# Performance work log

Hardware: AMD Instinct MI355X
Metric: run time of the kernel (lower is better)

Reference implementation:

```python
import jax, jax.numpy as jnp
import numpy as np

D = 256; NH = 8; NL = 4; NP = 4; DH = D // NH; DFFN = 1024; NQ = 900; BS = 4
SPATIAL = ((92, 92), (46, 46), (23, 23), (12, 12))  # (H, W) per level
LEVEL_START = (0, 8464, 10580, 11109)
S = sum(h * w for h, w in SPATIAL)  # 11253


def _ln(x, g, b):
    m = jnp.mean(x, -1, keepdims=True)
    v = jnp.var(x, -1, keepdims=True)
    return (x - m) / jnp.sqrt(v + 1e-5) * g + b


def setup_inputs() -> dict:
    key = jax.random.key(0)
    ks = jax.random.split(key, 24)
    p = lambda k, s: 0.02 * jax.random.normal(k, s, jnp.float32)
    return {
        "tgt": jax.random.normal(ks[0], (NQ, BS, D), jnp.float32),
        "tgt_query_pos": jax.random.normal(ks[1], (NQ, BS, D), jnp.float32),
        "tgt_reference_points": jax.random.uniform(ks[2], (NQ, BS, NL, 2), jnp.float32),
        "memory": jax.random.normal(ks[3], (S, BS, D), jnp.float32),
        "memory_spatial_shapes": jnp.array(SPATIAL, jnp.int32),
        "memory_level_start_index": jnp.array(LEVEL_START, jnp.int32),
        "in_proj_w": p(ks[4], (3 * D, D)), "in_proj_b": p(ks[5], (3 * D,)),
        "out_proj_w": p(ks[6], (D, D)), "out_proj_b": p(ks[7], (D,)),
        "off_w": p(ks[8], (NH * NL * NP * 2, D)), "off_b": p(ks[9], (NH * NL * NP * 2,)),
        "aw_w": p(ks[10], (NH * NL * NP, D)), "aw_b": p(ks[11], (NH * NL * NP,)),
        "vproj_w": p(ks[12], (D, D)), "vproj_b": p(ks[13], (D,)),
        "oproj_w": p(ks[14], (D, D)), "oproj_b": p(ks[15], (D,)),
        "ln1_g": jnp.ones((D,), jnp.float32), "ln1_b": jnp.zeros((D,), jnp.float32),
        "ln2_g": jnp.ones((D,), jnp.float32), "ln2_b": jnp.zeros((D,), jnp.float32),
        "ln3_g": jnp.ones((D,), jnp.float32), "ln3_b": jnp.zeros((D,), jnp.float32),
        "lin1_w": p(ks[16], (DFFN, D)), "lin1_b": p(ks[17], (DFFN,)),
        "lin2_w": p(ks[18], (D, DFFN)), "lin2_b": p(ks[19], (D,)),
    }


def _self_attn(q, k, v, in_w, in_b, out_w, out_b):
    # q, k, v: (nq, bs, d) -- torch nn.MultiheadAttention, eval mode
    wq, wk, wv = jnp.split(in_w, 3, axis=0)
    bq, bk, bv = jnp.split(in_b, 3)
    qp = (q @ wq.T + bq).reshape(NQ, BS, NH, DH)
    kp = (k @ wk.T + bk).reshape(NQ, BS, NH, DH)
    vp = (v @ wv.T + bv).reshape(NQ, BS, NH, DH)
    s = jnp.einsum("qbhd,kbhd->bhqk", qp, kp) / jnp.sqrt(jnp.float32(DH))
    a = jax.nn.softmax(s, axis=-1)
    o = jnp.einsum("bhqk,kbhd->qbhd", a, vp).reshape(NQ, BS, D)
    return o @ out_w.T + out_b


def _msdeform(x, ref, mem, off_w, off_b, aw_w, aw_b, vproj_w, vproj_b, oproj_w, oproj_b):
    # x: (bs, nq, d); ref: (bs, nq, nl, 2) in [0,1]; mem: (bs, S, d)
    value = (mem @ vproj_w.T + vproj_b).reshape(BS, S, NH, DH)
    off = (x @ off_w.T + off_b).reshape(BS, NQ, NH, NL, NP, 2)
    aw = jax.nn.softmax((x @ aw_w.T + aw_b).reshape(BS, NQ, NH, NL * NP), axis=-1)
    aw = aw.reshape(BS, NQ, NH, NL, NP)
    # offset normalizer = (W, H) per level
    norm = jnp.array([[w, h] for (h, w) in SPATIAL], jnp.float32)
    loc = ref[:, :, None, :, None, :] + off / norm[None, None, None, :, None, :]
    out = jnp.zeros((BS, NH, NQ, DH), x.dtype)
    for l, (H, W) in enumerate(SPATIAL):
        s0 = LEVEL_START[l]
        v = value[:, s0:s0 + H * W].transpose(0, 2, 1, 3)  # (bs, nh, H*W, dh)
        g = loc[:, :, :, l].transpose(0, 2, 1, 3, 4)       # (bs, nh, nq, np, 2)
        # grid_sample align_corners=False, padding_mode='zeros'
        px = g[..., 0] * W - 0.5
        py = g[..., 1] * H - 0.5
        x0 = jnp.floor(px).astype(jnp.int32)
        y0 = jnp.floor(py).astype(jnp.int32)
        wx = px - x0
        wy = py - y0
        samp = jnp.zeros((BS, NH, NQ, NP, DH), x.dtype)
        for dx, dy, w in ((0, 0, (1 - wx) * (1 - wy)), (1, 0, wx * (1 - wy)),
                          (0, 1, (1 - wx) * wy), (1, 1, wx * wy)):
            xi = x0 + dx
            yi = y0 + dy
            valid = ((xi >= 0) & (xi < W) & (yi >= 0) & (yi < H)).astype(x.dtype)
            idx = (jnp.clip(yi, 0, H - 1) * W + jnp.clip(xi, 0, W - 1)).reshape(BS, NH, NQ * NP)
            gat = jnp.take_along_axis(v, idx[..., None], axis=2).reshape(BS, NH, NQ, NP, DH)
            samp = samp + (w * valid)[..., None] * gat
        a = aw[:, :, :, l].transpose(0, 2, 1, 3)  # (bs, nh, nq, np)
        out = out + (samp * a[..., None]).sum(axis=3)
    out = out.transpose(0, 2, 1, 3).reshape(BS, NQ, D)
    return out @ oproj_w.T + oproj_b


def reference(tgt, tgt_query_pos, tgt_reference_points, memory,
              memory_spatial_shapes, memory_level_start_index,
              in_proj_w, in_proj_b, out_proj_w, out_proj_b,
              off_w, off_b, aw_w, aw_b, vproj_w, vproj_b, oproj_w, oproj_b,
              ln1_g, ln1_b, ln2_g, ln2_b, ln3_g, ln3_b,
              lin1_w, lin1_b, lin2_w, lin2_b):
    # module_seq = ['sa', 'ca', 'ffn']; dropout inactive (eval)
    q = tgt + tgt_query_pos
    tgt2 = _self_attn(q, q, tgt, in_proj_w, in_proj_b, out_proj_w, out_proj_b)
    tgt = _ln(tgt + tgt2, ln2_g, ln2_b)
    x = (tgt + tgt_query_pos).transpose(1, 0, 2)
    ref = tgt_reference_points.transpose(1, 0, 2, 3)
    mem = memory.transpose(1, 0, 2)
    tgt2 = _msdeform(x, ref, mem, off_w, off_b, aw_w, aw_b,
                     vproj_w, vproj_b, oproj_w, oproj_b).transpose(1, 0, 2)
    tgt = _ln(tgt + tgt2, ln1_g, ln1_b)
    ff = jax.nn.relu(tgt @ lin1_w.T + lin1_b) @ lin2_w.T + lin2_b
    return _ln(tgt + ff, ln3_g, ln3_b)
```

## Files before the change

### kernel.cpp

```cpp
#include <hip/hip_runtime.h>
#include <math.h>

#define D_MODEL 256
#define NHEAD   8
#define NLVL    4
#define NPTS    4
#define DHEAD   32
#define DFFN    1024
#define NQ      900
#define BSZ     4
#define NROW    (NQ * BSZ)
#define S_TOT   11253
#define VROWS   (S_TOT * BSZ)
#define SASCALE 0.17677669529663687f

typedef __attribute__((ext_vector_type(8))) short short8;
typedef __attribute__((ext_vector_type(4))) float f32x4;
typedef unsigned short ushort_t;

static __device__ __forceinline__ unsigned f2bf1(float f) {
    unsigned u = __float_as_uint(f);
    return (u + 0x7FFFu + ((u >> 16) & 1u)) >> 16;
}
static __device__ __forceinline__ unsigned pack2bf(float x, float y) {
    return f2bf1(x) | (f2bf1(y) << 16);
}
static __device__ __forceinline__ float bf2f(ushort_t u) {
    return __uint_as_float(((unsigned)u) << 16);
}

#define GPAD 72

#define WB_IN   0
#define WB_VP   196608
#define WB_OUTP 262144
#define WB_OFF  327680
#define WB_AW   393216
#define WB_OP   425984
#define WB_L1   491520
#define WB_L2   753664
#define WB_TOT  1015808

__global__ __launch_bounds__(256) void cvt_weights(
    const float* __restrict__ w_in, const float* __restrict__ w_vp,
    const float* __restrict__ w_outp, const float* __restrict__ w_off,
    const float* __restrict__ w_aw, const float* __restrict__ w_op,
    const float* __restrict__ w_l1, const float* __restrict__ w_l2,
    ushort_t* __restrict__ dst)
{
    int b = blockIdx.x;
    const float* src;
    int dstoff;
    if (b < 96)       { src = w_in;   dstoff = WB_IN;   }
    else if (b < 128) { src = w_vp;   b -= 96;  dstoff = WB_VP;   }
    else if (b < 160) { src = w_outp; b -= 128; dstoff = WB_OUTP; }
    else if (b < 192) { src = w_off;  b -= 160; dstoff = WB_OFF;  }
    else if (b < 208) { src = w_aw;   b -= 192; dstoff = WB_AW;   }
    else if (b < 240) { src = w_op;   b -= 208; dstoff = WB_OP;   }
    else if (b < 368) { src = w_l1;   b -= 240; dstoff = WB_L1;   }
    else              { src = w_l2;   b -= 368; dstoff = WB_L2;   }
    int i = (b * 256 + threadIdx.x) * 8;
    float4 f0 = *(const float4*)(src + i);
    float4 f1 = *(const float4*)(src + i + 4);
    uint4 u;
    u.x = pack2bf(f0.x, f0.y); u.y = pack2bf(f0.z, f0.w);
    u.z = pack2bf(f1.x, f1.y); u.w = pack2bf(f1.z, f1.w);
    *(uint4*)(dst + dstoff + i) = u;
}

__global__ __launch_bounds__(256) void proj_fused(
    const float* __restrict__ tgt, const float* __restrict__ qpos,
    const ushort_t* __restrict__ in_wb, const float* __restrict__ in_b,
    const float* __restrict__ mem, const ushort_t* __restrict__ vp_wb,
    const float* __restrict__ vp_b,
    ushort_t* __restrict__ qkv16, ushort_t* __restrict__ value16)
{
    __shared__ ushort_t As[64 * GPAD];
    __shared__ ushort_t Ws[128 * GPAD];

    const int t    = threadIdx.x;
    const int bid  = blockIdx.x;
    const int trow = t >> 2;
    const int tk   = (t & 3) << 4;
    const int wv   = t >> 6;
    const int ln   = t & 63;
    const int L    = ln & 15;
    const int quad = ln >> 4;

    if (bid < 684) {
        const int m0 = (bid % 57) * 64;
        const int n0 = (bid / 57) * 64;
        const bool addpos = (n0 < 512);
        const float oscale = (n0 < 256) ? SASCALE : 1.f;

        const int  mrow = m0 + trow;
        const bool mv   = (mrow < NROW);
        const float* arow = tgt  + (size_t)mrow * 256 + tk;
        const float* prow = qpos + (size_t)mrow * 256 + tk;
        const ushort_t* wrow = in_wb + (size_t)(n0 + trow) * 256 + tk;

        f32x4 acc[4] = {{0.f,0.f,0.f,0.f},{0.f,0.f,0.f,0.f},
                        {0.f,0.f,0.f,0.f},{0.f,0.f,0.f,0.f}};

        for (int k0 = 0; k0 < 256; k0 += 64) {
            uint4 u0, u1;
            if (mv) {
                const float* ap = arow + k0;
                float4 a0 = *(const float4*)(ap + 0);
                float4 a1 = *(const float4*)(ap + 4);
                float4 a2 = *(const float4*)(ap + 8);
                float4 a3 = *(const float4*)(ap + 12);
                if (addpos) {
                    const float* pp = prow + k0;
                    float4 p0 = *(const float4*)(pp + 0);
                    float4 p1 = *(const float4*)(pp + 4);
                    float4 p2 = *(const float4*)(pp + 8);
                    float4 p3 = *(const float4*)(pp + 12);
                    a0.x += p0.x; a0.y += p0.y; a0.z += p0.z; a0.w += p0.w;
                    a1.x += p1.x; a1.y += p1.y; a1.z += p1.z; a1.w += p1.w;
                    a2.x += p2.x; a2.y += p2.y; a2.z += p2.z; a2.w += p2.w;
                    a3.x += p3.x; a3.y += p3.y; a3.z += p3.z; a3.w += p3.w;
                }
                u0.x = pack2bf(a0.x, a0.y); u0.y = pack2bf(a0.z, a0.w);
                u0.z = pack2bf(a1.x, a1.y); u0.w = pack2bf(a1.z, a1.w);
                u1.x = pack2bf(a2.x, a2.y); u1.y = pack2bf(a2.z, a2.w);
                u1.z = pack2bf(a3.x, a3.y); u1.w = pack2bf(a3.z, a3.w);
            } else {
                u0 = make_uint4(0u, 0u, 0u, 0u); u1 = u0;
            }
            *(uint4*)&As[trow * GPAD + tk + 0] = u0;
            *(uint4*)&As[trow * GPAD + tk + 8] = u1;
            {
                const ushort_t* wp = wrow + k0;
                *(uint4*)&Ws[trow * GPAD + tk + 0] = *(const uint4*)(wp + 0);
                *(uint4*)&Ws[trow * GPAD + tk + 8] = *(const uint4*)(wp + 8);
            }
            __syncthreads();
#pragma unroll
            for (int kh = 0; kh < 2; ++kh) {
                short8 af = *(const short8*)&As[(wv * 16 + L) * GPAD + kh * 32 + quad * 8];
#pragma unroll
                for (int cb = 0; cb < 4; ++cb) {
                    short8 bf = *(const short8*)&Ws[(cb * 16 + L) * GPAD + kh * 32 + quad * 8];
                    acc[cb] = __builtin_amdgcn_mfma_f32_16x16x32_bf16(af, bf, acc[cb], 0, 0, 0);
                }
            }
            __syncthreads();
        }
#pragma unroll
        for (int cb = 0; cb < 4; ++cb) {
            int col = n0 + cb * 16 + L;
            float bv = in_b[col];
#pragma unroll
            for (int i = 0; i < 4; ++i) {
                int m = m0 + wv * 16 + quad * 4 + i;
                if (m < NROW)
                    qkv16[(size_t)m * 768 + col] = (ushort_t)f2bf1((acc[cb][i] + bv) * oscale);
            }
        }
    } else {
        const int vb = bid - 684;
        const int m0 = vb * 64;

        const int  mrow = m0 + trow;
        const bool mv   = (mrow < VROWS);
        const float* arow = mem + (size_t)mrow * 256 + tk;

        f32x4 acc[16];
#pragma unroll
        for (int i = 0; i < 16; ++i) acc[i] = (f32x4){0.f, 0.f, 0.f, 0.f};

        for (int k0 = 0; k0 < 256; k0 += 64) {
            uint4 u0, u1;
            if (mv) {
                const float* ap = arow + k0;
                float4 a0 = *(const float4*)(ap + 0);
                float4 a1 = *(const float4*)(ap + 4);
                float4 a2 = *(const float4*)(ap + 8);
                float4 a3 = *(const float4*)(ap + 12);
                u0.x = pack2bf(a0.x, a0.y); u0.y = pack2bf(a0.z, a0.w);
                u0.z = pack2bf(a1.x, a1.y); u0.w = pack2bf(a1.z, a1.w);
                u1.x = pack2bf(a2.x, a2.y); u1.y = pack2bf(a2.z, a2.w);
                u1.z = pack2bf(a3.x, a3.y); u1.w = pack2bf(a3.z, a3.w);
            } else {
                u0 = make_uint4(0u, 0u, 0u, 0u); u1 = u0;
            }
            *(uint4*)&As[trow * GPAD + tk + 0] = u0;
            *(uint4*)&As[trow * GPAD + tk + 8] = u1;
#pragma unroll
            for (int wg = 0; wg < 2; ++wg) {
                int n = wg * 64 + trow;
                const ushort_t* wp = vp_wb + (size_t)n * 256 + k0 + tk;
                *(uint4*)&Ws[n * GPAD + tk + 0] = *(const uint4*)(wp + 0);
                *(uint4*)&Ws[n * GPAD + tk + 8] = *(const uint4*)(wp + 8);
            }
            __syncthreads();
#pragma unroll
            for (int kh = 0; kh < 2; ++kh) {
                short8 af = *(const short8*)&As[(wv * 16 + L) * GPAD + kh * 32 + quad * 8];
#pragma unroll
                for (int cb = 0; cb < 8; ++cb) {
                    short8 bf = *(const short8*)&Ws[(cb * 16 + L) * GPAD + kh * 32 + quad * 8];
                    acc[cb] = __builtin_amdgcn_mfma_f32_16x16x32_bf16(af, bf, acc[cb], 0, 0, 0);
                }
            }
            __syncthreads();
#pragma unroll
            for (int wg = 0; wg < 2; ++wg) {
                int n = wg * 64 + trow;
                const ushort_t* wp = vp_wb + (size_t)(128 + n) * 256 + k0 + tk;
                *(uint4*)&Ws[n * GPAD + tk + 0] = *(const uint4*)(wp + 0);
                *(uint4*)&Ws[n * GPAD + tk + 8] = *(const uint4*)(wp + 8);
            }
            __syncthreads();
#pragma unroll
            for (int kh = 0; kh < 2; ++kh) {
                short8 af = *(const short8*)&As[(wv * 16 + L) * GPAD + kh * 32 + quad * 8];
#pragma unroll
                for (int cb = 0; cb < 8; ++cb) {
                    short8 bf = *(const short8*)&Ws[(cb * 16 + L) * GPAD + kh * 32 + quad * 8];
                    acc[8 + cb] = __builtin_amdgcn_mfma_f32_16x16x32_bf16(af, bf, acc[8 + cb], 0, 0, 0);
                }
            }
            __syncthreads();
        }

        ushort_t* Cs = Ws;
#pragma unroll
        for (int half = 0; half < 2; ++half) {
            if (half) __syncthreads();
#pragma unroll
            for (int cb = 0; cb < 8; ++cb) {
                int col = cb * 16 + L;
                float bv = vp_b[half * 128 + col];
#pragma unroll
                for (int i = 0; i < 4; ++i) {
                    int r = wv * 16 + quad * 4 + i;
                    Cs[r * 136 + col] = (ushort_t)f2bf1(acc[half * 8 + cb][i] + bv);
                }
            }
            __syncthreads();
            {
                int r  = t >> 2;
                int ch = (t & 3) * 32;
                int m  = m0 + r;
                if (m < VROWS) {
                    const ushort_t* src = &Cs[r * 136 + ch];
                    uint4* dst = (uint4*)(value16 + (size_t)m * 256 + half * 128 + ch);
#pragma unroll
                    for (int j = 0; j < 4; ++j)
                        dst[j] = *(const uint4*)(src + j * 8);
                }
            }
        }
    }
}

__global__ __launch_bounds__(256) void sa_flash16(
    const ushort_t* __restrict__ qkv, ushort_t* __restrict__ attn_out)
{
    __shared__ ushort_t Ks[2 * 2080];
    __shared__ ushort_t Vt[2 * 2304];
    __shared__ ushort_t Ps[4 * 1152];

    const int t    = threadIdx.x;
    const int q0   = blockIdx.x * 64;
    const int b    = blockIdx.y & 3;
    const int h    = blockIdx.y >> 2;
    const int wv   = t >> 6;
    const int ln   = t & 63;
    const int L    = ln & 15;
    const int quad = ln >> 4;

    union { uint4 u; short8 s; } qu;
    qu.u = make_uint4(0u, 0u, 0u, 0u);
    {
        int q = q0 + wv * 16 + L;
        if (q < NQ)
            qu.u = *(const uint4*)(qkv + ((size_t)q * 4 + b) * 768 + h * 32 + quad * 8);
    }
    const short8 qf = qu.s;

    float mrun = -1e30f, lrun = 0.f;
    f32x4 oacc[2] = {{0.f,0.f,0.f,0.f},{0.f,0.f,0.f,0.f}};

    const int skey = t >> 2;
    const int sdg  = t & 3;

    uint4 ku, vu;
    auto kv_load = [&](int k0) {
        int kg = k0 + skey;
        ku = make_uint4(0u, 0u, 0u, 0u);
        vu = make_uint4(0u, 0u, 0u, 0u);
        if (kg < NQ) {
            const ushort_t* base = qkv + ((size_t)kg * 4 + b) * 768 + 256 + h * 32 + sdg * 8;
            ku = *(const uint4*)base;
            vu = *(const uint4*)(base + 256);
        }
    };

    kv_load(0);
    int it = 0;
    for (int k0 = 0; k0 < NQ; k0 += 64, it ^= 1) {
        *(uint4*)&Ks[it * 2080 + sdg * 520 + skey * 8] = ku;
        {
            ushort_t* vp = &Vt[it * 2304 + sdg * 8 * 72 + skey];
            vp[0 * 72] = (ushort_t)(vu.x & 0xffffu);
            vp[1 * 72] = (ushort_t)(vu.x >> 16);
            vp[2 * 72] = (ushort_t)(vu.y & 0xffffu);
            vp[3 * 72] = (ushort_t)(vu.y >> 16);
            vp[4 * 72] = (ushort_t)(vu.z & 0xffffu);
            vp[5 * 72] = (ushort_t)(vu.z >> 16);
            vp[6 * 72] = (ushort_t)(vu.w & 0xffffu);
            vp[7 * 72] = (ushort_t)(vu.w >> 16);
        }
        __syncthreads();
        if (k0 + 64 < NQ) kv_load(k0 + 64);

        f32x4 sacc[4] = {{0.f,0.f,0.f,0.f},{0.f,0.f,0.f,0.f},
                         {0.f,0.f,0.f,0.f},{0.f,0.f,0.f,0.f}};
#pragma unroll
        for (int cb = 0; cb < 4; ++cb) {
            short8 kf = *(const short8*)&Ks[it * 2080 + quad * 520 + (cb * 16 + L) * 8];
            sacc[cb] = __builtin_amdgcn_mfma_f32_16x16x32_bf16(kf, qf, sacc[cb], 0, 0, 0);
        }
        if (k0 + 64 > NQ) {
#pragma unroll
            for (int cb = 0; cb < 4; ++cb)
#pragma unroll
                for (int i = 0; i < 4; ++i)
                    if (k0 + cb * 16 + quad * 4 + i >= NQ) sacc[cb][i] = -1e30f;
        }

        float ml = -1e30f;
#pragma unroll
        for (int cb = 0; cb < 4; ++cb)
#pragma unroll
            for (int i = 0; i < 4; ++i) ml = fmaxf(ml, sacc[cb][i]);
        ml = fmaxf(ml, __shfl_xor(ml, 16, 64));
        ml = fmaxf(ml, __shfl_xor(ml, 32, 64));
        float mnew  = fmaxf(mrun, ml);
        float alpha = __expf(mrun - mnew);
        float p[16];
        float rs = 0.f;
#pragma unroll
        for (int cb = 0; cb < 4; ++cb)
#pragma unroll
            for (int i = 0; i < 4; ++i) {
                float e = __expf(sacc[cb][i] - mnew);
                p[cb * 4 + i] = e;
                rs += e;
            }
        rs += __shfl_xor(rs, 16, 64);
        rs += __shfl_xor(rs, 32, 64);
        lrun = lrun * alpha + rs;
        mrun = mnew;

        {
            ushort_t* pw = &Ps[wv * 1152 + L * 72];
#pragma unroll
            for (int cb = 0; cb < 4; ++cb) {
                uint2 u;
                u.x = pack2bf(p[cb * 4 + 0], p[cb * 4 + 1]);
                u.y = pack2bf(p[cb * 4 + 2], p[cb * 4 + 3]);
                *(uint2*)&pw[cb * 16 + quad * 4] = u;
            }
        }
#pragma unroll
        for (int i = 0; i < 4; ++i) {
            float ai = __shfl(alpha, quad * 4 + i, 64);
            oacc[0][i] *= ai;
            oacc[1][i] *= ai;
        }
        __syncthreads();

#pragma unroll
        for (int ks = 0; ks < 2; ++ks) {
            short8 pf = *(const short8*)&Ps[wv * 1152 + L * 72 + ks * 32 + quad * 8];
#pragma unroll
            for (int db = 0; db < 2; ++db) {
                short8 vf = *(const short8*)&Vt[it * 2304 + (db * 16 + L) * 72 + ks * 32 + quad * 8];
                oacc[db] = __builtin_amdgcn_mfma_f32_16x16x32_bf16(pf, vf, oacc[db], 0, 0, 0);
            }
        }
    }

#pragma unroll
    for (int i = 0; i < 4; ++i) {
        float lq = __shfl(lrun, quad * 4 + i, 64);
        float li = 1.f / lq;
        int q = q0 + wv * 16 + quad * 4 + i;
        if (q < NQ) {
            ushort_t* op = attn_out + ((size_t)q * 4 + b) * 256 + h * 32 + L;
            op[0]  = (ushort_t)f2bf1(oacc[0][i] * li);
            op[16] = (ushort_t)f2bf1(oacc[1][i] * li);
        }
    }
}

__global__ __launch_bounds__(256) void gemm_ln16(
    const ushort_t* __restrict__ A, const ushort_t* __restrict__ W,
    const float* __restrict__ bias, const float* __restrict__ resid,
    const float* __restrict__ gam, const float* __restrict__ bet,
    float* __restrict__ out, const float* __restrict__ pos,
    ushort_t* __restrict__ out2, int M, int K)
{
    __shared__ ushort_t As[16 * GPAD];
    __shared__ ushort_t Ws[256 * GPAD];
    __shared__ float sS[4][16];
    __shared__ float s2S[4][16];

    const int t  = threadIdx.x;
    const int m0 = blockIdx.x * 16;
    const int trow = t >> 2;
    const int tk   = (t & 3) << 4;
    const int wv   = t >> 6;
    const int ln   = t & 63;
    const int L    = ln & 15;
    const int quad = ln >> 4;

    f32x4 acc[4] = {{0.f,0.f,0.f,0.f},{0.f,0.f,0.f,0.f},
                    {0.f,0.f,0.f,0.f},{0.f,0.f,0.f,0.f}};

    for (int k0 = 0; k0 < K; k0 += 64) {
        if (t < 128) {
            int r = t >> 3, seg = (t & 7) * 8;
            int m = m0 + r;
            uint4 a = make_uint4(0u, 0u, 0u, 0u);
            if (m < M) a = *(const uint4*)(A + (size_t)m * K + k0 + seg);
            *(uint4*)&As[r * GPAD + seg] = a;
        }
#pragma unroll
        for (int wg = 0; wg < 4; ++wg) {
            int n = wg * 64 + trow;
            const ushort_t* wp = W + (size_t)n * K + k0 + tk;
            *(uint4*)&Ws[n * GPAD + tk + 0] = *(const uint4*)(wp + 0);
            *(uint4*)&Ws[n * GPAD + tk + 8] = *(const uint4*)(wp + 8);
        }
        __syncthreads();
#pragma unroll
        for (int kh = 0; kh < 2; ++kh) {
            short8 af = *(const short8*)&As[L * GPAD + kh * 32 + quad * 8];
#pragma unroll
            for (int cb = 0; cb < 4; ++cb) {
                short8 bf = *(const short8*)&Ws[(wv * 64 + cb * 16 + L) * GPAD + kh * 32 + quad * 8];
                acc[cb] = __builtin_amdgcn_mfma_f32_16x16x32_bf16(af, bf, acc[cb], 0, 0, 0);
            }
        }
        __syncthreads();
    }

    float s[4]  = {0.f, 0.f, 0.f, 0.f};
    float s2[4] = {0.f, 0.f, 0.f, 0.f};
#pragma unroll
    for (int cb = 0; cb < 4; ++cb) {
        int col = wv * 64 + cb * 16 + L;
        float bv = bias[col];
#pragma unroll
        for (int i = 0; i < 4; ++i) {
            int m = m0 + quad * 4 + i;
            float r = (m < M) ? resid[(size_t)m * 256 + col] : 0.f;
            float xv = acc[cb][i] + bv + r;
            acc[cb][i] = xv;
            s[i]  += xv;
            s2[i] += xv * xv;
        }
    }
#pragma unroll
    for (int off = 1; off < 16; off <<= 1) {
#pragma unroll
        for (int i = 0; i < 4; ++i) {
            s[i]  += __shfl_xor(s[i],  off, 64);
            s2[i] += __shfl_xor(s2[i], off, 64);
        }
    }
    if (L == 0) {
#pragma unroll
        for (int i = 0; i < 4; ++i) {
            sS[wv][quad * 4 + i]  = s[i];
            s2S[wv][quad * 4 + i] = s2[i];
        }
    }
    __syncthreads();
    float mean[4], rstd[4];
#pragma unroll
    for (int i = 0; i < 4; ++i) {
        int row = quad * 4 + i;
        float St  = sS[0][row]  + sS[1][row]  + sS[2][row]  + sS[3][row];
        float S2t = s2S[0][row] + s2S[1][row] + s2S[2][row] + s2S[3][row];
        mean[i] = St * (1.f / 256.f);
        float var = S2t * (1.f / 256.f) - mean[i] * mean[i];
        rstd[i] = rsqrtf(var + 1e-5f);
    }
#pragma unroll
    for (int cb = 0; cb < 4; ++cb) {
        int col = wv * 64 + cb * 16 + L;
        float gv = gam[col];
        float bt = bet[col];
#pragma unroll
        for (int i = 0; i < 4; ++i) {
            int m = m0 + quad * 4 + i;
            if (m < M) {
                float y = (acc[cb][i] - mean[i]) * rstd[i] * gv + bt;
                out[(size_t)m * 256 + col] = y;
                if (out2) {
                    float o2 = y + (pos ? pos[(size_t)m * 256 + col] : 0.f);
                    out2[(size_t)m * 256 + col] = (ushort_t)f2bf1(o2);
                }
            }
        }
    }
}

__global__ __launch_bounds__(256) void offaw16(
    const ushort_t* __restrict__ A,
    const ushort_t* __restrict__ off_wb, const float* __restrict__ off_b,
    const ushort_t* __restrict__ aw_wb, const float* __restrict__ aw_b,
    float* __restrict__ off_raw, float* __restrict__ aw_raw)
{
    __shared__ ushort_t As[64 * GPAD];
    __shared__ ushort_t Ws[64 * GPAD];

    const int t  = threadIdx.x;
    const int m0 = blockIdx.x * 64;
    const int by = blockIdx.y;
    const bool isaw = (by >= 4);
    const int n0 = isaw ? (by - 4) * 64 : by * 64;
    const ushort_t* W = isaw ? aw_wb : off_wb;
    const float* bs = isaw ? aw_b : off_b;
    float* C = isaw ? aw_raw : off_raw;
    const int ldc = isaw ? 128 : 256;

    const int trow = t >> 2;
    const int tk   = (t & 3) << 4;
    const int wv   = t >> 6;
    const int ln   = t & 63;
    const int L    = ln & 15;
    const int quad = ln >> 4;

    const int  mrow = m0 + trow;
    const bool mv   = (mrow < NROW);
    const ushort_t* arow = A + (size_t)mrow * 256 + tk;
    const ushort_t* wrow = W + (size_t)(n0 + trow) * 256 + tk;

    f32x4 acc[4] = {{0.f,0.f,0.f,0.f},{0.f,0.f,0.f,0.f},
                    {0.f,0.f,0.f,0.f},{0.f,0.f,0.f,0.f}};

    for (int k0 = 0; k0 < 256; k0 += 64) {
        {
            uint4 a0 = make_uint4(0u,0u,0u,0u), a1 = a0;
            if (mv) {
                a0 = *(const uint4*)(arow + k0);
                a1 = *(const uint4*)(arow + k0 + 8);
            }
            *(uint4*)&As[trow * GPAD + tk + 0] = a0;
            *(uint4*)&As[trow * GPAD + tk + 8] = a1;
        }
        {
            const ushort_t* wp = wrow + k0;
            *(uint4*)&Ws[trow * GPAD + tk + 0] = *(const uint4*)(wp + 0);
            *(uint4*)&Ws[trow * GPAD + tk + 8] = *(const uint4*)(wp + 8);
        }
        __syncthreads();
#pragma unroll
        for (int kh = 0; kh < 2; ++kh) {
            short8 af = *(const short8*)&As[(wv * 16 + L) * GPAD + kh * 32 + quad * 8];
#pragma unroll
            for (int cb = 0; cb < 4; ++cb) {
                short8 bf = *(const short8*)&Ws[(cb * 16 + L) * GPAD + kh * 32 + quad * 8];
                acc[cb] = __builtin_amdgcn_mfma_f32_16x16x32_bf16(af, bf, acc[cb], 0, 0, 0);
            }
        }
        __syncthreads();
    }
#pragma unroll
    for (int cb = 0; cb < 4; ++cb) {
        int col = n0 + cb * 16 + L;
        float bv = bs[col];
#pragma unroll
        for (int i = 0; i < 4; ++i) {
            int m = m0 + wv * 16 + quad * 4 + i;
            if (m < NROW)
                C[(size_t)m * ldc + col] = acc[cb][i] + bv;
        }
    }
}

__global__ __launch_bounds__(256) void gemm16_16(
    const ushort_t* __restrict__ A, const ushort_t* __restrict__ W,
    const float* __restrict__ bias, ushort_t* __restrict__ C,
    int M, int N, int K, int ldc, int relu)
{
    __shared__ ushort_t As[64 * GPAD];
    __shared__ ushort_t Ws[64 * GPAD];

    const int t  = threadIdx.x;
    const int m0 = blockIdx.x * 64;
    const int n0 = blockIdx.y * 64;
    const int trow = t >> 2;
    const int tk   = (t & 3) << 4;
    const int wv   = t >> 6;
    const int ln   = t & 63;
    const int L    = ln & 15;
    const int quad = ln >> 4;

    const int  mrow = m0 + trow;
    const bool mv   = (mrow < M);
    const ushort_t* arow = A + (size_t)mrow * K + tk;
    const ushort_t* wrow = W + (size_t)(n0 + trow) * K + tk;

    f32x4 acc[4] = {{0.f,0.f,0.f,0.f},{0.f,0.f,0.f,0.f},
                    {0.f,0.f,0.f,0.f},{0.f,0.f,0.f,0.f}};

    for (int k0 = 0; k0 < K; k0 += 64) {
        {
            uint4 a0 = make_uint4(0u,0u,0u,0u), a1 = a0;
            if (mv) {
                a0 = *(const uint4*)(arow + k0);
                a1 = *(const uint4*)(arow + k0 + 8);
            }
            *(uint4*)&As[trow * GPAD + tk + 0] = a0;
            *(uint4*)&As[trow * GPAD + tk + 8] = a1;
        }
        {
            const ushort_t* wp = wrow + k0;
            *(uint4*)&Ws[trow * GPAD + tk + 0] = *(const uint4*)(wp + 0);
            *(uint4*)&Ws[trow * GPAD + tk + 8] = *(const uint4*)(wp + 8);
        }
        __syncthreads();
#pragma unroll
        for (int kh = 0; kh < 2; ++kh) {
            short8 af = *(const short8*)&As[(wv * 16 + L) * GPAD + kh * 32 + quad * 8];
#pragma unroll
            for (int cb = 0; cb < 4; ++cb) {
                short8 bf = *(const short8*)&Ws[(cb * 16 + L) * GPAD + kh * 32 + quad * 8];
                acc[cb] = __builtin_amdgcn_mfma_f32_16x16x32_bf16(af, bf, acc[cb], 0, 0, 0);
            }
        }
        __syncthreads();
    }
#pragma unroll
    for (int cb = 0; cb < 4; ++cb) {
        int col = n0 + cb * 16 + L;
        float bv = bias[col];
#pragma unroll
        for (int i = 0; i < 4; ++i) {
            int m = m0 + wv * 16 + quad * 4 + i;
            if (m < M) {
                float o = acc[cb][i] + bv;
                if (relu) o = fmaxf(o, 0.f);
                C[(size_t)m * ldc + col] = (ushort_t)f2bf1(o);
            }
        }
    }
}

__global__ __launch_bounds__(256) void msdeform16(
    const float* __restrict__ off_raw, const float* __restrict__ aw_raw,
    const float* __restrict__ refp, const ushort_t* __restrict__ value,
    ushort_t* __restrict__ out)
{
    const int row = blockIdx.x;
    const int b = row & 3;
    const int t = threadIdx.x;

    __shared__ float aw_s[8][17];
    __shared__ float px_s[8][16];
    __shared__ float py_s[8][16];

    const int Hs[4]  = {92, 46, 23, 12};
    const int Wd[4]  = {92, 46, 23, 12};
    const int S0_[4] = {0, 8464, 10580, 11109};

    if (t < 128) {
        int hh = t >> 4, lp = t & 15, l = lp >> 2;
        float ox = off_raw[(size_t)row * 256 + hh * 32 + lp * 2 + 0];
        float oy = off_raw[(size_t)row * 256 + hh * 32 + lp * 2 + 1];
        float rx = refp[((size_t)row * 4 + l) * 2 + 0];
        float ry = refp[((size_t)row * 4 + l) * 2 + 1];
        px_s[hh][lp] = rx * (float)Wd[l] + ox - 0.5f;
        py_s[hh][lp] = ry * (float)Hs[l] + oy - 0.5f;
    }
    if (t < 8) {
        int hh = t;
        float v[16];
        float m = -1e30f;
#pragma unroll
        for (int j = 0; j < 16; ++j) {
            v[j] = aw_raw[(size_t)row * 128 + hh * 16 + j];
            m = fmaxf(m, v[j]);
        }
        float ssum = 0.f;
#pragma unroll
        for (int j = 0; j < 16; ++j) { v[j] = __expf(v[j] - m); ssum += v[j]; }
        float inv = 1.f / ssum;
#pragma unroll
        for (int j = 0; j < 16; ++j) aw_s[hh][j] = v[j] * inv;
    }
    __syncthreads();

    const int h = t >> 5, d = t & 31;
    const ushort_t* vb = value + (size_t)b * 256 + h * 32 + d;
    float acc = 0.f;
#pragma unroll
    for (int l = 0; l < 4; ++l) {
        const int H = Hs[l], W = Wd[l], base = S0_[l];
#pragma unroll
        for (int p = 0; p < 4; ++p) {
            const int lp = l * 4 + p;
            float px = px_s[h][lp], py = py_s[h][lp];
            float x0f = floorf(px), y0f = floorf(py);
            int x0 = (int)x0f, y0 = (int)y0f;
            float wx = px - x0f, wy = py - y0f;
            float sv = 0.f;
#pragma unroll
            for (int dy = 0; dy < 2; ++dy) {
#pragma unroll
                for (int dx = 0; dx < 2; ++dx) {
                    int xi = x0 + dx, yi = y0 + dy;
                    float flag = (xi >= 0 && xi < W && yi >= 0 && yi < H) ? 1.f : 0.f;
                    int xc = xi < 0 ? 0 : (xi >= W ? W - 1 : xi);
                    int yc = yi < 0 ? 0 : (yi >= H ? H - 1 : yi);
                    float wgt = (dx ? wx : 1.f - wx) * (dy ? wy : 1.f - wy);
                    float gv = bf2f(vb[(size_t)(base + yc * W + xc) * 1024]);
                    sv = fmaf(wgt * flag, gv, sv);
                }
            }
            acc = fmaf(aw_s[h][lp], sv, acc);
        }
    }
    out[(size_t)row * 256 + h * 32 + d] = (ushort_t)f2bf1(acc);
}

extern "C" void kernel_launch(void* const* d_in, const int* in_sizes, int n_in,
                              void* d_out, int out_size, void* d_ws, size_t ws_size,
                              hipStream_t stream)
{
    const float* tgt    = (const float*)d_in[0];
    const float* qpos   = (const float*)d_in[1];
    const float* refp   = (const float*)d_in[2];
    const float* mem    = (const float*)d_in[3];
    const float* in_w   = (const float*)d_in[6];
    const float* in_b   = (const float*)d_in[7];
    const float* outp_w = (const float*)d_in[8];
    const float* outp_b = (const float*)d_in[9];
    const float* off_w  = (const float*)d_in[10];
    const float* off_b  = (const float*)d_in[11];
    const float* aw_w   = (const float*)d_in[12];
    const float* aw_b   = (const float*)d_in[13];
    const float* vp_w   = (const float*)d_in[14];
    const float* vp_b   = (const float*)d_in[15];
    const float* op_w   = (const float*)d_in[16];
    const float* op_b   = (const float*)d_in[17];
    const float* ln1g   = (const float*)d_in[18];
    const float* ln1b   = (const float*)d_in[19];
    const float* ln2g   = (const float*)d_in[20];
    const float* ln2b   = (const float*)d_in[21];
    const float* ln3g   = (const float*)d_in[22];
    const float* ln3b   = (const float*)d_in[23];
    const float* l1w    = (const float*)d_in[24];
    const float* l1b    = (const float*)d_in[25];
    const float* l2w    = (const float*)d_in[26];
    const float* l2b    = (const float*)d_in[27];
    float* out = (float*)d_out;
    float* ws  = (float*)d_ws;

    ushort_t* qkv16    = (ushort_t*)ws;
    ushort_t* att16    = (ushort_t*)(ws + 691200);
    float*    tgt_a    = ws + 1843200;
    ushort_t* xca16    = (ushort_t*)(ws + 2764800);
    float*    off_raw  = ws + 2995200;
    float*    aw_raw   = ws + 3916800;
    ushort_t* att2_16  = (ushort_t*)(ws + 4377600);
    float*    tgt_b    = ws + 4608000;
    ushort_t* tgtb16   = (ushort_t*)(ws + 5529600);
    ushort_t* value16  = (ushort_t*)(ws + 5760000);
    ushort_t* hidden16 = (ushort_t*)(ws + 11521536);
    ushort_t* wb       = (ushort_t*)(ws + 13364736);

    const ushort_t* in_wb   = wb + WB_IN;
    const ushort_t* vp_wb   = wb + WB_VP;
    const ushort_t* outp_wb = wb + WB_OUTP;
    const ushort_t* off_wb  = wb + WB_OFF;
    const ushort_t* aw_wb   = wb + WB_AW;
    const ushort_t* op_wb   = wb + WB_OP;
    const ushort_t* l1_wb   = wb + WB_L1;
    const ushort_t* l2_wb   = wb + WB_L2;

    dim3 b256(256);

    hipLaunchKernelGGL(cvt_weights, dim3(496), b256, 0, stream,
                       in_w, vp_w, outp_w, off_w, aw_w, op_w, l1w, l2w, wb);
    hipLaunchKernelGGL(proj_fused, dim3(1388), b256, 0, stream,
                       tgt, qpos, in_wb, in_b, mem, vp_wb, vp_b, qkv16, value16);
    hipLaunchKernelGGL(sa_flash16, dim3(15, 32), b256, 0, stream, qkv16, att16);
    hipLaunchKernelGGL(gemm_ln16, dim3(225), b256, 0, stream,
                       att16, outp_wb, outp_b, tgt, ln2g, ln2b,
                       tgt_a, qpos, xca16, NROW, 256);
    hipLaunchKernelGGL(offaw16, dim3(57, 6), b256, 0, stream,
                       xca16, off_wb, off_b, aw_wb, aw_b, off_raw, aw_raw);
    hipLaunchKernelGGL(msdeform16, dim3(3600), b256, 0, stream,
                       off_raw, aw_raw, refp, value16, att2_16);
    hipLaunchKernelGGL(gemm_ln16, dim3(225), b256, 0, stream,
                       att2_16, op_wb, op_b, tgt_a, ln1g, ln1b,
                       tgt_b, (const float*)nullptr, tgtb16, NROW, 256);
    hipLaunchKernelGGL(gemm16_16, dim3(57, 16), b256, 0, stream,
                       tgtb16, l1_wb, l1b, hidden16, NROW, 1024, 256, 1024, 1);
    hipLaunchKernelGGL(gemm_ln16, dim3(225), b256, 0, stream,
                       hidden16, l2_wb, l2b, tgt_b, ln3g, ln3b,
                       out, (const float*)nullptr, (ushort_t*)nullptr, NROW, 1024);
}
```

Before: 276.2 us.

## Stage bf16 weights via direct global-to-LDS loads with XOR-swizzled layout

```diff
diff --git a/kernel.cpp b/kernel.cpp
--- a/kernel.cpp
+++ b/kernel.cpp
@@ -31,6 +31,21 @@
 
 #define GPAD 72
 
+#if __has_builtin(__builtin_amdgcn_global_load_lds)
+#define HAS_GLL 1
+#endif
+
+static __device__ __forceinline__ void stage_w16(const ushort_t* g, ushort_t* ldsbase, int lane)
+{
+#ifdef HAS_GLL
+    __builtin_amdgcn_global_load_lds(
+        (const __attribute__((address_space(1))) unsigned int*)g,
+        (__attribute__((address_space(3))) unsigned int*)ldsbase, 16, 0, 0);
+#else
+    *(uint4*)(ldsbase + lane * 8) = *(const uint4*)g;
+#endif
+}
+
 #define WB_IN   0
 #define WB_VP   196608
 #define WB_OUTP 262144
@@ -51,6 +66,7 @@
     int b = blockIdx.x;
     const float* src;
     int dstoff;
+    int kbits = 8;
     if (b < 96)       { src = w_in;   dstoff = WB_IN;   }
     else if (b < 128) { src = w_vp;   b -= 96;  dstoff = WB_VP;   }
     else if (b < 160) { src = w_outp; b -= 128; dstoff = WB_OUTP; }
@@ -58,14 +74,18 @@
     else if (b < 208) { src = w_aw;   b -= 192; dstoff = WB_AW;   }
     else if (b < 240) { src = w_op;   b -= 208; dstoff = WB_OP;   }
     else if (b < 368) { src = w_l1;   b -= 240; dstoff = WB_L1;   }
-    else              { src = w_l2;   b -= 368; dstoff = WB_L2;   }
+    else              { src = w_l2;   b -= 368; dstoff = WB_L2;   kbits = 10; }
     int i = (b * 256 + threadIdx.x) * 8;
     float4 f0 = *(const float4*)(src + i);
     float4 f1 = *(const float4*)(src + i + 4);
     uint4 u;
     u.x = pack2bf(f0.x, f0.y); u.y = pack2bf(f0.z, f0.w);
     u.z = pack2bf(f1.x, f1.y); u.w = pack2bf(f1.z, f1.w);
-    *(uint4*)(dst + dstoff + i) = u;
+    int K = 1 << kbits;
+    int n = i >> kbits;
+    int k = i & (K - 1);
+    int kswz = (k & ~63) | ((k & 63) ^ ((n & 7) << 3));
+    *(uint4*)(dst + dstoff + (size_t)n * K + kswz) = u;
 }
 
 __global__ __launch_bounds__(256) void proj_fused(
@@ -76,7 +96,7 @@
     ushort_t* __restrict__ qkv16, ushort_t* __restrict__ value16)
 {
     __shared__ ushort_t As[64 * GPAD];
-    __shared__ ushort_t Ws[128 * GPAD];
+    __shared__ ushort_t Ws[8704];
 
     const int t    = threadIdx.x;
     const int bid  = blockIdx.x;
@@ -86,6 +106,9 @@
     const int ln   = t & 63;
     const int L    = ln & 15;
     const int quad = ln >> 4;
+    const int swz  = (L & 7) << 3;
+    const int lrow = ln >> 3;
+    const int lchk = (ln & 7) << 3;
 
     if (bid < 684) {
         const int m0 = (bid % 57) * 64;
@@ -97,12 +120,17 @@
         const bool mv   = (mrow < NROW);
         const float* arow = tgt  + (size_t)mrow * 256 + tk;
         const float* prow = qpos + (size_t)mrow * 256 + tk;
-        const ushort_t* wrow = in_wb + (size_t)(n0 + trow) * 256 + tk;
 
         f32x4 acc[4] = {{0.f,0.f,0.f,0.f},{0.f,0.f,0.f,0.f},
                         {0.f,0.f,0.f,0.f},{0.f,0.f,0.f,0.f}};
 
         for (int k0 = 0; k0 < 256; k0 += 64) {
+#pragma unroll
+            for (int j = 0; j < 2; ++j) {
+                int r0 = (wv * 2 + j) * 8;
+                const ushort_t* g = in_wb + (size_t)(n0 + r0 + lrow) * 256 + k0 + lchk;
+                stage_w16(g, &Ws[r0 * 64], ln);
+            }
             uint4 u0, u1;
             if (mv) {
                 const float* ap = arow + k0;
@@ -130,18 +158,13 @@
             }
             *(uint4*)&As[trow * GPAD + tk + 0] = u0;
             *(uint4*)&As[trow * GPAD + tk + 8] = u1;
-            {
-                const ushort_t* wp = wrow + k0;
-                *(uint4*)&Ws[trow * GPAD + tk + 0] = *(const uint4*)(wp + 0);
-                *(uint4*)&Ws[trow * GPAD + tk + 8] = *(const uint4*)(wp + 8);
-            }
             __syncthreads();
 #pragma unroll
             for (int kh = 0; kh < 2; ++kh) {
                 short8 af = *(const short8*)&As[(wv * 16 + L) * GPAD + kh * 32 + quad * 8];
 #pragma unroll
                 for (int cb = 0; cb < 4; ++cb) {
-                    short8 bf = *(const short8*)&Ws[(cb * 16 + L) * GPAD + kh * 32 + quad * 8];
+                    short8 bf = *(const short8*)&Ws[(cb * 16 + L) * 64 + ((kh * 32 + quad * 8) ^ swz)];
                     acc[cb] = __builtin_amdgcn_mfma_f32_16x16x32_bf16(af, bf, acc[cb], 0, 0, 0);
                 }
             }
@@ -171,6 +194,12 @@
         for (int i = 0; i < 16; ++i) acc[i] = (f32x4){0.f, 0.f, 0.f, 0.f};
 
         for (int k0 = 0; k0 < 256; k0 += 64) {
+#pragma unroll
+            for (int j = 0; j < 4; ++j) {
+                int r0 = (wv * 4 + j) * 8;
+                const ushort_t* g = vp_wb + (size_t)(r0 + lrow) * 256 + k0 + lchk;
+                stage_w16(g, &Ws[r0 * 64], ln);
+            }
             uint4 u0, u1;
             if (mv) {
                 const float* ap = arow + k0;
@@ -187,30 +216,22 @@
             }
             *(uint4*)&As[trow * GPAD + tk + 0] = u0;
             *(uint4*)&As[trow * GPAD + tk + 8] = u1;
-#pragma unroll
-            for (int wg = 0; wg < 2; ++wg) {
-                int n = wg * 64 + trow;
-                const ushort_t* wp = vp_wb + (size_t)n * 256 + k0 + tk;
-                *(uint4*)&Ws[n * GPAD + tk + 0] = *(const uint4*)(wp + 0);
-                *(uint4*)&Ws[n * GPAD + tk + 8] = *(const uint4*)(wp + 8);
-            }
             __syncthreads();
 #pragma unroll
             for (int kh = 0; kh < 2; ++kh) {
                 short8 af = *(const short8*)&As[(wv * 16 + L) * GPAD + kh * 32 + quad * 8];
 #pragma unroll
                 for (int cb = 0; cb < 8; ++cb) {
-                    short8 bf = *(const short8*)&Ws[(cb * 16 + L) * GPAD + kh * 32 + quad * 8];
+                    short8 bf = *(const short8*)&Ws[(cb * 16 + L) * 64 + ((kh * 32 + quad * 8) ^ swz)];
                     acc[cb] = __builtin_amdgcn_mfma_f32_16x16x32_bf16(af, bf, acc[cb], 0, 0, 0);
                 }
             }
             __syncthreads();
 #pragma unroll
-            for (int wg = 0; wg < 2; ++wg) {
-                int n = wg * 64 + trow;
-                const ushort_t* wp = vp_wb + (size_t)(128 + n) * 256 + k0 + tk;
-                *(uint4*)&Ws[n * GPAD + tk + 0] = *(const uint4*)(wp + 0);
-                *(uint4*)&Ws[n * GPAD + tk + 8] = *(const uint4*)(wp + 8);
+            for (int j = 0; j < 4; ++j) {
+                int r0 = (wv * 4 + j) * 8;
+                const ushort_t* g = vp_wb + (size_t)(128 + r0 + lrow) * 256 + k0 + lchk;
+                stage_w16(g, &Ws[r0 * 64], ln);
             }
             __syncthreads();
 #pragma unroll
@@ -218,7 +239,7 @@
                 short8 af = *(const short8*)&As[(wv * 16 + L) * GPAD + kh * 32 + quad * 8];
 #pragma unroll
                 for (int cb = 0; cb < 8; ++cb) {
-                    short8 bf = *(const short8*)&Ws[(cb * 16 + L) * GPAD + kh * 32 + quad * 8];
+                    short8 bf = *(const short8*)&Ws[(cb * 16 + L) * 64 + ((kh * 32 + quad * 8) ^ swz)];
                     acc[8 + cb] = __builtin_amdgcn_mfma_f32_16x16x32_bf16(af, bf, acc[8 + cb], 0, 0, 0);
                 }
             }
@@ -406,23 +427,30 @@
     ushort_t* __restrict__ out2, int M, int K)
 {
     __shared__ ushort_t As[16 * GPAD];
-    __shared__ ushort_t Ws[256 * GPAD];
+    __shared__ ushort_t Ws[256 * 64];
     __shared__ float sS[4][16];
     __shared__ float s2S[4][16];
 
     const int t  = threadIdx.x;
     const int m0 = blockIdx.x * 16;
-    const int trow = t >> 2;
-    const int tk   = (t & 3) << 4;
     const int wv   = t >> 6;
     const int ln   = t & 63;
     const int L    = ln & 15;
     const int quad = ln >> 4;
+    const int swz  = (L & 7) << 3;
+    const int lrow = ln >> 3;
+    const int lchk = (ln & 7) << 3;
 
     f32x4 acc[4] = {{0.f,0.f,0.f,0.f},{0.f,0.f,0.f,0.f},
                     {0.f,0.f,0.f,0.f},{0.f,0.f,0.f,0.f}};
 
     for (int k0 = 0; k0 < K; k0 += 64) {
+#pragma unroll
+        for (int j = 0; j < 8; ++j) {
+            int r0 = (wv * 8 + j) * 8;
+            const ushort_t* g = W + (size_t)(r0 + lrow) * K + k0 + lchk;
+            stage_w16(g, &Ws[r0 * 64], ln);
+        }
         if (t < 128) {
             int r = t >> 3, seg = (t & 7) * 8;
             int m = m0 + r;
@@ -430,20 +458,13 @@
             if (m < M) a = *(const uint4*)(A + (size_t)m * K + k0 + seg);
             *(uint4*)&As[r * GPAD + seg] = a;
         }
-#pragma unroll
-        for (int wg = 0; wg < 4; ++wg) {
-            int n = wg * 64 + trow;
-            const ushort_t* wp = W + (size_t)n * K + k0 + tk;
-            *(uint4*)&Ws[n * GPAD + tk + 0] = *(const uint4*)(wp + 0);
-            *(uint4*)&Ws[n * GPAD + tk + 8] = *(const uint4*)(wp + 8);
-        }
         __syncthreads();
 #pragma unroll
         for (int kh = 0; kh < 2; ++kh) {
             short8 af = *(const short8*)&As[L * GPAD + kh * 32 + quad * 8];
 #pragma unroll
             for (int cb = 0; cb < 4; ++cb) {
-                short8 bf = *(const short8*)&Ws[(wv * 64 + cb * 16 + L) * GPAD + kh * 32 + quad * 8];
+                short8 bf = *(const short8*)&Ws[(wv * 64 + cb * 16 + L) * 64 + ((kh * 32 + quad * 8) ^ swz)];
                 acc[cb] = __builtin_amdgcn_mfma_f32_16x16x32_bf16(af, bf, acc[cb], 0, 0, 0);
             }
         }
@@ -519,7 +540,7 @@
     float* __restrict__ off_raw, float* __restrict__ aw_raw)
 {
     __shared__ ushort_t As[64 * GPAD];
-    __shared__ ushort_t Ws[64 * GPAD];
+    __shared__ ushort_t Ws[64 * 64];
 
     const int t  = threadIdx.x;
     const int m0 = blockIdx.x * 64;
@@ -537,16 +558,24 @@
     const int ln   = t & 63;
     const int L    = ln & 15;
     const int quad = ln >> 4;
+    const int swz  = (L & 7) << 3;
+    const int lrow = ln >> 3;
+    const int lchk = (ln & 7) << 3;
 
     const int  mrow = m0 + trow;
     const bool mv   = (mrow < NROW);
     const ushort_t* arow = A + (size_t)mrow * 256 + tk;
-    const ushort_t* wrow = W + (size_t)(n0 + trow) * 256 + tk;
 
     f32x4 acc[4] = {{0.f,0.f,0.f,0.f},{0.f,0.f,0.f,0.f},
                     {0.f,0.f,0.f,0.f},{0.f,0.f,0.f,0.f}};
 
     for (int k0 = 0; k0 < 256; k0 += 64) {
+#pragma unroll
+        for (int j = 0; j < 2; ++j) {
+            int r0 = (wv * 2 + j) * 8;
+            const ushort_t* g = W + (size_t)(n0 + r0 + lrow) * 256 + k0 + lchk;
+            stage_w16(g, &Ws[r0 * 64], ln);
+        }
         {
             uint4 a0 = make_uint4(0u,0u,0u,0u), a1 = a0;
             if (mv) {
@@ -556,18 +585,13 @@
             *(uint4*)&As[trow * GPAD + tk + 0] = a0;
             *(uint4*)&As[trow * GPAD + tk + 8] = a1;
         }
-        {
-            const ushort_t* wp = wrow + k0;
-            *(uint4*)&Ws[trow * GPAD + tk + 0] = *(const uint4*)(wp + 0);
-            *(uint4*)&Ws[trow * GPAD + tk + 8] = *(const uint4*)(wp + 8);
-        }
         __syncthreads();
 #pragma unroll
         for (int kh = 0; kh < 2; ++kh) {
             short8 af = *(const short8*)&As[(wv * 16 + L) * GPAD + kh * 32 + quad * 8];
 #pragma unroll
             for (int cb = 0; cb < 4; ++cb) {
-                short8 bf = *(const short8*)&Ws[(cb * 16 + L) * GPAD + kh * 32 + quad * 8];
+                short8 bf = *(const short8*)&Ws[(cb * 16 + L) * 64 + ((kh * 32 + quad * 8) ^ swz)];
                 acc[cb] = __builtin_amdgcn_mfma_f32_16x16x32_bf16(af, bf, acc[cb], 0, 0, 0);
             }
         }
@@ -592,7 +616,7 @@
     int M, int N, int K, int ldc, int relu)
 {
     __shared__ ushort_t As[64 * GPAD];
-    __shared__ ushort_t Ws[64 * GPAD];
+    __shared__ ushort_t Ws[64 * 64];
 
     const int t  = threadIdx.x;
     const int m0 = blockIdx.x * 64;
@@ -603,16 +627,24 @@
     const int ln   = t & 63;
     const int L    = ln & 15;
     const int quad = ln >> 4;
+    const int swz  = (L & 7) << 3;
+    const int lrow = ln >> 3;
+    const int lchk = (ln & 7) << 3;
 
     const int  mrow = m0 + trow;
     const bool mv   = (mrow < M);
     const ushort_t* arow = A + (size_t)mrow * K + tk;
-    const ushort_t* wrow = W + (size_t)(n0 + trow) * K + tk;
 
     f32x4 acc[4] = {{0.f,0.f,0.f,0.f},{0.f,0.f,0.f,0.f},
                     {0.f,0.f,0.f,0.f},{0.f,0.f,0.f,0.f}};
 
     for (int k0 = 0; k0 < K; k0 += 64) {
+#pragma unroll
+        for (int j = 0; j < 2; ++j) {
+            int r0 = (wv * 2 + j) * 8;
+            const ushort_t* g = W + (size_t)(n0 + r0 + lrow) * K + k0 + lchk;
+            stage_w16(g, &Ws[r0 * 64], ln);
+        }
         {
             uint4 a0 = make_uint4(0u,0u,0u,0u), a1 = a0;
             if (mv) {
@@ -622,18 +654,13 @@
             *(uint4*)&As[trow * GPAD + tk + 0] = a0;
             *(uint4*)&As[trow * GPAD + tk + 8] = a1;
         }
-        {
-            const ushort_t* wp = wrow + k0;
-            *(uint4*)&Ws[trow * GPAD + tk + 0] = *(const uint4*)(wp + 0);
-            *(uint4*)&Ws[trow * GPAD + tk + 8] = *(const uint4*)(wp + 8);
-        }
         __syncthreads();
 #pragma unroll
         for (int kh = 0; kh < 2; ++kh) {
             short8 af = *(const short8*)&As[(wv * 16 + L) * GPAD + kh * 32 + quad * 8];
 #pragma unroll
             for (int cb = 0; cb < 4; ++cb) {
-                short8 bf = *(const short8*)&Ws[(cb * 16 + L) * GPAD + kh * 32 + quad * 8];
+                short8 bf = *(const short8*)&Ws[(cb * 16 + L) * 64 + ((kh * 32 + quad * 8) ^ swz)];
                 acc[cb] = __builtin_amdgcn_mfma_f32_16x16x32_bf16(af, bf, acc[cb], 0, 0, 0);
             }
         }
```

Measured after the change: 267.0 us. 1.03x faster.
